# Performance work log

Measured on AMD Instinct MI355X. Metric: run time of the kernel, lower is better.

Reference implementation:

```python
import jax, jax.numpy as jnp
import numpy as np

EPS = 1e-20

def setup_inputs() -> dict:
    key = jax.random.key(0)
    k1, k2, k3, k4, k5 = jax.random.split(key, 5)
    B, S, E, D = 8, 2048, 1024, 1024
    x = jax.random.normal(k1, (B, S, E), dtype=jnp.float32)
    mask = jax.random.randint(k2, (B, S, S), 0, 2, dtype=jnp.int32)
    scale = 1.0 / np.sqrt(E)
    Wq = jax.random.normal(k3, (E, D), dtype=jnp.float32) * scale
    Wk = jax.random.normal(k4, (E, D), dtype=jnp.float32) * scale
    Wv = jax.random.normal(k5, (E, D), dtype=jnp.float32) * scale
    return {"x": x, "mask": mask, "Wq": Wq, "Wk": Wk, "Wv": Wv}

def masked_softmax(scores, mask, axis=-1):
    # non-standard: multiply scores by mask BEFORE softmax, re-mask, renormalize
    w = jax.nn.softmax(scores * mask, axis=axis)
    w = w * mask
    return w / (w.sum(axis, keepdims=True) + EPS)

def reference(x, mask, Wq, Wk, Wv):
    D = Wq.shape[1]
    m = mask.astype(x.dtype)                       # [B,S,S]
    q = jnp.einsum('bse,ed->bsd', x, Wq)
    k = jnp.einsum('bse,ed->bsd', x, Wk)
    v = jnp.einsum('bse,ed->bsd', x, Wv)
    scores = jnp.einsum('bqd,bkd->bqk', q, k) / jnp.sqrt(jnp.asarray(D, x.dtype))
    attn = masked_softmax(scores, m, axis=-1)      # [B,S,S]
    return jnp.einsum('bqk,bkd->bqd', attn, v)
```

## Files before the change

### kernel.cpp

```cpp
#include <hip/hip_runtime.h>
#include <hip/hip_bf16.h>

#define S_LEN 2048
#define E_DIM 1024
#define D_DIM 1024

typedef __bf16 bf16x8 __attribute__((ext_vector_type(8)));
typedef __bf16 bf16x4 __attribute__((ext_vector_type(4)));
typedef float f32x4 __attribute__((ext_vector_type(4)));

__device__ __forceinline__ __bf16 f2bf(float f) {
    unsigned u = __builtin_bit_cast(unsigned, f);
    u += 0x7fffu + ((u >> 16) & 1u);
    unsigned short h = (unsigned short)(u >> 16);
    return __builtin_bit_cast(__bf16, h);
}

__device__ __forceinline__ void async_cp16(void* lds, const void* g) {
    __builtin_amdgcn_global_load_lds(
        (const __attribute__((address_space(1))) void*)g,
        (__attribute__((address_space(3))) void*)lds, 16, 0, 0);
}

#define MFMA_BLOCK()                                                              \
    _Pragma("unroll")                                                             \
    for (int kk = 0; kk < 2; ++kk) {                                              \
        const int kb = kk * 64 + lh * 16;                                         \
        bf16x8 a[4], b[4];                                                        \
        _Pragma("unroll")                                                         \
        for (int m = 0; m < 4; ++m)                                               \
            a[m] = *reinterpret_cast<const bf16x8*>(lsA + (wr*64 + m*16 + rl) * 128 + kb); \
        _Pragma("unroll")                                                         \
        for (int n = 0; n < 4; ++n)                                               \
            b[n] = *reinterpret_cast<const bf16x8*>(lsB + (wc*64 + n*16 + rl) * 128 + kb); \
        _Pragma("unroll")                                                         \
        for (int m = 0; m < 4; ++m)                                               \
            _Pragma("unroll")                                                     \
            for (int n = 0; n < 4; ++n)                                           \
                acc[m][n] = __builtin_amdgcn_mfma_f32_16x16x32_bf16(a[m], b[n], acc[m][n], 0, 0, 0); \
    }

#define STAGE_TILE(lsDst, gBase, row0, kcol, stride)                              \
    _Pragma("unroll")                                                             \
    for (int i_ = 0; i_ < 4; ++i_) {                                              \
        int r_ = wid * 32 + i_ * 8;                                               \
        async_cp16(lsDst + r_ * 128,                                              \
                   gBase + (size_t)((row0) + r_ + lrow) * (stride) + (kcol) + lcol); \
    }

__global__ __launch_bounds__(256) void cvt_x_kernel(
    const float* __restrict__ X, __bf16* __restrict__ Xb)
{
    const int n8 = (8 * S_LEN * E_DIM) / 8;
    for (int i = blockIdx.x * 256 + threadIdx.x; i < n8; i += gridDim.x * 256) {
        const float* p = X + (size_t)i * 8;
        float4 a = *reinterpret_cast<const float4*>(p);
        float4 b = *reinterpret_cast<const float4*>(p + 4);
        bf16x8 h = { f2bf(a.x), f2bf(a.y), f2bf(a.z), f2bf(a.w),
                     f2bf(b.x), f2bf(b.y), f2bf(b.z), f2bf(b.w) };
        *reinterpret_cast<bf16x8*>(Xb + (size_t)i * 8) = h;
    }
}

__global__ __launch_bounds__(256) void wt_kernel(
    const float* __restrict__ Wq, const float* __restrict__ Wk, const float* __restrict__ Wv,
    __bf16* __restrict__ Wt)
{
    __shared__ float t[64][68];
    const int z = blockIdx.z;
    const float* W = (z == 0) ? Wq : (z == 1) ? Wk : Wv;
    const int d0 = blockIdx.x * 64, e0 = blockIdx.y * 64;
    const int tid = threadIdx.x;

    const int er = tid >> 4, dc = (tid & 15) * 4;
    #pragma unroll
    for (int p = 0; p < 4; ++p) {
        int e = p * 16 + er;
        float4 v = *reinterpret_cast<const float4*>(W + (size_t)(e0 + e) * D_DIM + d0 + dc);
        *reinterpret_cast<float4*>(&t[e][dc]) = v;
    }
    __syncthreads();

    const int dl = tid >> 3, ec = (tid & 7) * 8;
    __bf16* O = Wt + (size_t)z * E_DIM * D_DIM;
    #pragma unroll
    for (int p = 0; p < 2; ++p) {
        int d = p * 32 + dl;
        bf16x8 h;
        #pragma unroll
        for (int j = 0; j < 8; ++j) h[j] = f2bf(t[ec + j][d]);
        *reinterpret_cast<bf16x8*>(O + (size_t)(d0 + d) * E_DIM + e0 + ec) = h;
    }
}

__global__ __launch_bounds__(256) void qkv_kernel(
    const __bf16* __restrict__ Xb, const __bf16* __restrict__ Wt,
    __bf16* __restrict__ Qb, __bf16* __restrict__ Kb, __bf16* __restrict__ Vt)
{
    __shared__ __align__(16) char lsA[128 * 128];
    __shared__ __align__(16) char lsB[128 * 128];

    const int nt = blockIdx.x, mt = blockIdx.y, z = blockIdx.z;
    const __bf16* A  = Xb;
    const __bf16* Bm = Wt + (size_t)z * E_DIM * D_DIM;
    const int m0 = mt * 128, n0 = nt * 128;
    const int tid = threadIdx.x, lane = tid & 63, wid = tid >> 6;
    const int wr = wid >> 1, wc = wid & 1;
    const int rl = lane & 15, lh = lane >> 4;
    const int lrow = lane >> 3, lcol = (lane & 7) * 8;

    f32x4 acc[4][4] = {};

    for (int k0 = 0; k0 < E_DIM; k0 += 64) {
        STAGE_TILE(lsA, A,  m0, k0, E_DIM)
        STAGE_TILE(lsB, Bm, n0, k0, E_DIM)
        __syncthreads();
        MFMA_BLOCK()
        __syncthreads();
    }

    if (z < 2) {
        __bf16* O = (z == 0) ? Qb : Kb;
        #pragma unroll
        for (int m = 0; m < 4; ++m) {
            int row = m0 + wr*64 + m*16 + lh*4;
            #pragma unroll
            for (int n = 0; n < 4; ++n) {
                int col = n0 + wc*64 + n*16 + rl;
                #pragma unroll
                for (int r = 0; r < 4; ++r)
                    O[(size_t)(row + r) * D_DIM + col] = f2bf(acc[m][n][r]);
            }
        }
    } else {
        const int bz = m0 >> 11;
        const int srow = m0 & 2047;
        __bf16* O = Vt + (size_t)bz * D_DIM * S_LEN;
        #pragma unroll
        for (int m = 0; m < 4; ++m) {
            int row = srow + wr*64 + m*16 + lh*4;
            #pragma unroll
            for (int n = 0; n < 4; ++n) {
                int col = n0 + wc*64 + n*16 + rl;
                bf16x4 h = { f2bf(acc[m][n][0]), f2bf(acc[m][n][1]),
                             f2bf(acc[m][n][2]), f2bf(acc[m][n][3]) };
                *reinterpret_cast<bf16x4*>(O + (size_t)col * S_LEN + row) = h;
            }
        }
    }
}

__global__ __launch_bounds__(256) void qk_kernel(
    const __bf16* __restrict__ Qb, const __bf16* __restrict__ Kb,
    const int* __restrict__ mask, __bf16* __restrict__ P, float* __restrict__ rowsum)
{
    __shared__ __align__(16) char lsA[128 * 128];
    __shared__ __align__(16) char lsB[128 * 128];

    const int kt = blockIdx.x, qt = blockIdx.y, bz = blockIdx.z;
    const __bf16* A  = Qb + (size_t)bz * S_LEN * D_DIM;
    const __bf16* Bm = Kb + (size_t)bz * S_LEN * D_DIM;
    const int q0 = qt * 128, k0 = kt * 128;
    const int tid = threadIdx.x, lane = tid & 63, wid = tid >> 6;
    const int wr = wid >> 1, wc = wid & 1;
    const int rl = lane & 15, lh = lane >> 4;
    const int lrow = lane >> 3, lcol = (lane & 7) * 8;

    f32x4 acc[4][4] = {};

    for (int d0 = 0; d0 < D_DIM; d0 += 64) {
        STAGE_TILE(lsA, A,  q0, d0, D_DIM)
        STAGE_TILE(lsB, Bm, k0, d0, D_DIM)
        __syncthreads();
        MFMA_BLOCK()
        __syncthreads();
    }

    float rs[4][4] = {};
    const size_t mbase = (size_t)bz * S_LEN * S_LEN;
    #pragma unroll
    for (int m = 0; m < 4; ++m) {
        int row = q0 + wr*64 + m*16 + lh*4;
        #pragma unroll
        for (int n = 0; n < 4; ++n) {
            int col = k0 + wc*64 + n*16 + rl;
            #pragma unroll
            for (int r = 0; r < 4; ++r) {
                float s = acc[m][n][r] * 0.03125f;
                int mk = mask[mbase + (size_t)(row + r) * S_LEN + col];
                float pv = mk ? __expf(s) : 0.0f;
                rs[m][r] += pv;
                P[mbase + (size_t)(row + r) * S_LEN + col] = f2bf(pv);
            }
        }
    }
    #pragma unroll
    for (int m = 0; m < 4; ++m) {
        #pragma unroll
        for (int r = 0; r < 4; ++r) {
            float v = rs[m][r];
            v += __shfl_xor(v, 1);
            v += __shfl_xor(v, 2);
            v += __shfl_xor(v, 4);
            v += __shfl_xor(v, 8);
            if (rl == 0)
                atomicAdd(&rowsum[bz * S_LEN + q0 + wr*64 + m*16 + lh*4 + r], v);
        }
    }
}

__global__ __launch_bounds__(256) void pv_kernel(
    const __bf16* __restrict__ P, const __bf16* __restrict__ Vt,
    const float* __restrict__ rowsum, float* __restrict__ out)
{
    __shared__ __align__(16) char lsA[128 * 128];
    __shared__ __align__(16) char lsB[128 * 128];

    const int dt = blockIdx.x, qt = blockIdx.y, bz = blockIdx.z;
    const __bf16* A  = P  + (size_t)bz * S_LEN * S_LEN;
    const __bf16* Bv = Vt + (size_t)bz * D_DIM * S_LEN;
    const int q0 = qt * 128, d0c = dt * 128;
    const int tid = threadIdx.x, lane = tid & 63, wid = tid >> 6;
    const int wr = wid >> 1, wc = wid & 1;
    const int rl = lane & 15, lh = lane >> 4;
    const int lrow = lane >> 3, lcol = (lane & 7) * 8;

    f32x4 acc[4][4] = {};

    for (int s0 = 0; s0 < S_LEN; s0 += 64) {
        STAGE_TILE(lsA, A,  q0,  s0, S_LEN)
        STAGE_TILE(lsB, Bv, d0c, s0, S_LEN)
        __syncthreads();
        MFMA_BLOCK()
        __syncthreads();
    }

    float* Ob = out + (size_t)bz * S_LEN * D_DIM;
    #pragma unroll
    for (int m = 0; m < 4; ++m) {
        int row = q0 + wr*64 + m*16 + lh*4;
        float inv[4];
        #pragma unroll
        for (int r = 0; r < 4; ++r)
            inv[r] = 1.0f / (rowsum[bz * S_LEN + row + r] + 1e-20f);
        #pragma unroll
        for (int n = 0; n < 4; ++n) {
            int col = d0c + wc*64 + n*16 + rl;
            #pragma unroll
            for (int r = 0; r < 4; ++r)
                Ob[(size_t)(row + r) * D_DIM + col] = acc[m][n][r] * inv[r];
        }
    }
}

extern "C" void kernel_launch(void* const* d_in, const int* in_sizes, int n_in,
                              void* d_out, int out_size, void* d_ws, size_t ws_size,
                              hipStream_t stream) {
    const float* x    = (const float*)d_in[0];
    const int*   mask = (const int*)  d_in[1];
    const float* Wq   = (const float*)d_in[2];
    const float* Wk   = (const float*)d_in[3];
    const float* Wv   = (const float*)d_in[4];
    float* out = (float*)d_out;

    char* ws = (char*)d_ws;
    const size_t SZ_QKV = (size_t)8 * S_LEN * D_DIM * 2;
    const size_t SZ_P   = (size_t)8 * S_LEN * S_LEN * 2;
    __bf16* Qb = (__bf16*)(ws);
    __bf16* Kb = (__bf16*)(ws + SZ_QKV);
    __bf16* Vt = (__bf16*)(ws + 2 * SZ_QKV);
    char*   pbase = ws + 3 * SZ_QKV;
    __bf16* P  = (__bf16*)pbase;
    __bf16* Xb = (__bf16*)pbase;
    __bf16* Wt = (__bf16*)(pbase + (size_t)8 * S_LEN * E_DIM * 2);
    float* rowsum = (float*)(ws + 3 * SZ_QKV + SZ_P);
    const size_t need = 3 * SZ_QKV + SZ_P + (size_t)8 * S_LEN * 4;
    if (ws_size < need) return;

    hipMemsetAsync(rowsum, 0, (size_t)8 * S_LEN * 4, stream);
    cvt_x_kernel<<<2048, 256, 0, stream>>>(x, Xb);
    wt_kernel  <<<dim3(16, 16, 3), 256, 0, stream>>>(Wq, Wk, Wv, Wt);
    qkv_kernel <<<dim3(8, 128, 3), 256, 0, stream>>>(Xb, Wt, Qb, Kb, Vt);
    qk_kernel  <<<dim3(16, 16, 8), 256, 0, stream>>>(Qb, Kb, mask, P, rowsum);
    pv_kernel  <<<dim3(8, 16, 8),  256, 0, stream>>>(P, Vt, rowsum, out);
}
```

Before: 648.0 us.

## Use 256x256 double-buffered swizzled GEMM tiles with 512-thread blocks

Replaces the 128x128 single-buffered GEMM loop shared by the QKV, QK and PV kernels with a 256x256-tile, 8-wave routine. It double-buffers LDS across K-steps with async global-to-LDS loads, XOR-swizzles the LDS layout to avoid bank conflicts, and raises wave priority around the MFMA bursts. The aim is more data reuse per loaded byte and overlap of loads with matrix math. The cost is 128KB of LDS per block and 128 accumulator registers per thread, which may limit occupancy, and fewer blocks are launched, with possible tail effects.

```diff
diff --git a/kernel.cpp b/kernel.cpp
--- a/kernel.cpp
+++ b/kernel.cpp
@@ -16,37 +16,99 @@
     return __builtin_bit_cast(__bf16, h);
 }
 
+__device__ __forceinline__ int swz(int row, int b) {
+    return row * 128 + (b ^ ((row & 7) << 4));
+}
+
 __device__ __forceinline__ void async_cp16(void* lds, const void* g) {
     __builtin_amdgcn_global_load_lds(
         (const __attribute__((address_space(1))) void*)g,
         (__attribute__((address_space(3))) void*)lds, 16, 0, 0);
 }
 
-#define MFMA_BLOCK()                                                              \
-    _Pragma("unroll")                                                             \
-    for (int kk = 0; kk < 2; ++kk) {                                              \
-        const int kb = kk * 64 + lh * 16;                                         \
-        bf16x8 a[4], b[4];                                                        \
-        _Pragma("unroll")                                                         \
-        for (int m = 0; m < 4; ++m)                                               \
-            a[m] = *reinterpret_cast<const bf16x8*>(lsA + (wr*64 + m*16 + rl) * 128 + kb); \
-        _Pragma("unroll")                                                         \
-        for (int n = 0; n < 4; ++n)                                               \
-            b[n] = *reinterpret_cast<const bf16x8*>(lsB + (wc*64 + n*16 + rl) * 128 + kb); \
-        _Pragma("unroll")                                                         \
-        for (int m = 0; m < 4; ++m)                                               \
-            _Pragma("unroll")                                                     \
-            for (int n = 0; n < 4; ++n)                                           \
-                acc[m][n] = __builtin_amdgcn_mfma_f32_16x16x32_bf16(a[m], b[n], acc[m][n], 0, 0, 0); \
-    }
-
-#define STAGE_TILE(lsDst, gBase, row0, kcol, stride)                              \
-    _Pragma("unroll")                                                             \
-    for (int i_ = 0; i_ < 4; ++i_) {                                              \
-        int r_ = wid * 32 + i_ * 8;                                               \
-        async_cp16(lsDst + r_ * 128,                                              \
-                   gBase + (size_t)((row0) + r_ + lrow) * (stride) + (kcol) + lcol); \
-    }
+__device__ __forceinline__ void stage_q64(char* ldsTile, const char* gTile,
+                                          size_t strideB, int q, int tid)
+{
+    const int r   = q * 64 + (tid >> 3);
+    const int cb  = (tid & 7) * 16;
+    const int scb = cb ^ ((r & 7) << 4);
+    async_cp16(ldsTile + q * 8192 + ((tid >> 6) << 10),
+               gTile + (size_t)r * strideB + scb);
+}
+
+template<int QM, int QN>
+__device__ __forceinline__ void mfma_phase(const char* lsA, const char* lsB,
+    int wr, int wc, int rl, int lh, f32x4 (&acc)[8][4])
+{
+    bf16x8 a[4][2]; bf16x8 b[2][2];
+    #pragma unroll
+    for (int m = 0; m < 4; ++m)
+        #pragma unroll
+        for (int ks = 0; ks < 2; ++ks)
+            a[m][ks] = *reinterpret_cast<const bf16x8*>(
+                lsA + swz(wr*128 + QM*64 + m*16 + rl, ks*64 + lh*16));
+    #pragma unroll
+    for (int n = 0; n < 2; ++n)
+        #pragma unroll
+        for (int ks = 0; ks < 2; ++ks)
+            b[n][ks] = *reinterpret_cast<const bf16x8*>(
+                lsB + swz(wc*64 + QN*32 + n*16 + rl, ks*64 + lh*16));
+    __builtin_amdgcn_s_setprio(1);
+    #pragma unroll
+    for (int m = 0; m < 4; ++m)
+        #pragma unroll
+        for (int n = 0; n < 2; ++n)
+            #pragma unroll
+            for (int ks = 0; ks < 2; ++ks)
+                acc[QM*4+m][QN*2+n] = __builtin_amdgcn_mfma_f32_16x16x32_bf16(
+                    a[m][ks], b[n][ks], acc[QM*4+m][QN*2+n], 0, 0, 0);
+    __builtin_amdgcn_s_setprio(0);
+}
+
+__device__ __forceinline__ void gemm256(const char* gA, const char* gB,
+    size_t sA, size_t sB, int nt, char* ls, f32x4 (&acc)[8][4])
+{
+    const int tid = threadIdx.x, lane = tid & 63, wid = tid >> 6;
+    const int wr = wid >> 2, wc = wid & 3;
+    const int rl = lane & 15, lh = lane >> 4;
+    char* bA[2] = { ls,         ls + 65536 };
+    char* bB[2] = { ls + 32768, ls + 98304 };
+
+    #define STGA(t, q) stage_q64(bA[(t) & 1], gA + (size_t)(t) * 128, sA, q, tid)
+    #define STGB(t, q) stage_q64(bB[(t) & 1], gB + (size_t)(t) * 128, sB, q, tid)
+
+    STGA(0,0); STGA(0,1); STGA(0,2); STGA(0,3);
+    STGB(0,0); STGB(0,1); STGB(0,2); STGB(0,3);
+    STGA(1,0); STGA(1,2);
+    asm volatile("s_waitcnt vmcnt(2)" ::: "memory");
+    __builtin_amdgcn_s_barrier();
+    __builtin_amdgcn_sched_barrier(0);
+
+    for (int u = 0; u < nt; ++u) {
+        const char* lA = bA[u & 1]; const char* lB = bB[u & 1];
+        if (u + 1 < nt) {
+            STGA(u+1,1); STGA(u+1,3);
+            STGB(u+1,0); STGB(u+1,1); STGB(u+1,2); STGB(u+1,3);
+        }
+        mfma_phase<0,0>(lA, lB, wr, wc, rl, lh, acc);
+        mfma_phase<0,1>(lA, lB, wr, wc, rl, lh, acc);
+        __builtin_amdgcn_sched_barrier(0);
+        __builtin_amdgcn_s_barrier();
+        __builtin_amdgcn_sched_barrier(0);
+        if (u + 2 < nt) { STGA(u+2,0); STGA(u+2,2); }
+        mfma_phase<1,0>(lA, lB, wr, wc, rl, lh, acc);
+        mfma_phase<1,1>(lA, lB, wr, wc, rl, lh, acc);
+        if (u + 1 < nt) {
+            __builtin_amdgcn_sched_barrier(0);
+            if (u + 2 < nt) { asm volatile("s_waitcnt vmcnt(2)" ::: "memory"); }
+            else            { asm volatile("s_waitcnt vmcnt(0)" ::: "memory"); }
+            __builtin_amdgcn_s_barrier();
+            __builtin_amdgcn_sched_barrier(0);
+        }
+    }
+    #undef STGA
+    #undef STGB
+}
 
 __global__ __launch_bounds__(256) void cvt_x_kernel(
     const float* __restrict__ X, __bf16* __restrict__ Xb)
@@ -93,43 +155,34 @@
     }
 }
 
-__global__ __launch_bounds__(256) void qkv_kernel(
+__global__ __launch_bounds__(512, 2) void qkv_kernel(
     const __bf16* __restrict__ Xb, const __bf16* __restrict__ Wt,
     __bf16* __restrict__ Qb, __bf16* __restrict__ Kb, __bf16* __restrict__ Vt)
 {
-    __shared__ __align__(16) char lsA[128 * 128];
-    __shared__ __align__(16) char lsB[128 * 128];
-
-    const int nt = blockIdx.x, mt = blockIdx.y, z = blockIdx.z;
-    const __bf16* A  = Xb;
-    const __bf16* Bm = Wt + (size_t)z * E_DIM * D_DIM;
-    const int m0 = mt * 128, n0 = nt * 128;
+    __shared__ __align__(16) char ls[131072];
+    const int bx = blockIdx.x, mt = blockIdx.y, z = blockIdx.z;
+    const int m0 = mt * 256, n0 = bx * 256;
+
+    f32x4 acc[8][4] = {};
+    gemm256((const char*)Xb + (size_t)m0 * (E_DIM * 2),
+            (const char*)(Wt + (size_t)z * E_DIM * D_DIM) + (size_t)n0 * (E_DIM * 2),
+            E_DIM * 2, E_DIM * 2, E_DIM / 64, ls, acc);
+
     const int tid = threadIdx.x, lane = tid & 63, wid = tid >> 6;
-    const int wr = wid >> 1, wc = wid & 1;
+    const int wr = wid >> 2, wc = wid & 3;
     const int rl = lane & 15, lh = lane >> 4;
-    const int lrow = lane >> 3, lcol = (lane & 7) * 8;
-
-    f32x4 acc[4][4] = {};
-
-    for (int k0 = 0; k0 < E_DIM; k0 += 64) {
-        STAGE_TILE(lsA, A,  m0, k0, E_DIM)
-        STAGE_TILE(lsB, Bm, n0, k0, E_DIM)
-        __syncthreads();
-        MFMA_BLOCK()
-        __syncthreads();
-    }
 
     if (z < 2) {
         __bf16* O = (z == 0) ? Qb : Kb;
         #pragma unroll
-        for (int m = 0; m < 4; ++m) {
-            int row = m0 + wr*64 + m*16 + lh*4;
-            #pragma unroll
-            for (int n = 0; n < 4; ++n) {
-                int col = n0 + wc*64 + n*16 + rl;
+        for (int mi = 0; mi < 8; ++mi) {
+            int row = m0 + wr*128 + mi*16 + lh*4;
+            #pragma unroll
+            for (int ni = 0; ni < 4; ++ni) {
+                int col = n0 + wc*64 + ni*16 + rl;
                 #pragma unroll
                 for (int r = 0; r < 4; ++r)
-                    O[(size_t)(row + r) * D_DIM + col] = f2bf(acc[m][n][r]);
+                    O[(size_t)(row + r) * D_DIM + col] = f2bf(acc[mi][ni][r]);
             }
         }
     } else {
@@ -137,118 +190,100 @@
         const int srow = m0 & 2047;
         __bf16* O = Vt + (size_t)bz * D_DIM * S_LEN;
         #pragma unroll
-        for (int m = 0; m < 4; ++m) {
-            int row = srow + wr*64 + m*16 + lh*4;
-            #pragma unroll
-            for (int n = 0; n < 4; ++n) {
-                int col = n0 + wc*64 + n*16 + rl;
-                bf16x4 h = { f2bf(acc[m][n][0]), f2bf(acc[m][n][1]),
-                             f2bf(acc[m][n][2]), f2bf(acc[m][n][3]) };
+        for (int mi = 0; mi < 8; ++mi) {
+            int row = srow + wr*128 + mi*16 + lh*4;
+            #pragma unroll
+            for (int ni = 0; ni < 4; ++ni) {
+                int col = n0 + wc*64 + ni*16 + rl;
+                bf16x4 h = { f2bf(acc[mi][ni][0]), f2bf(acc[mi][ni][1]),
+                             f2bf(acc[mi][ni][2]), f2bf(acc[mi][ni][3]) };
                 *reinterpret_cast<bf16x4*>(O + (size_t)col * S_LEN + row) = h;
             }
         }
     }
 }
 
-__global__ __launch_bounds__(256) void qk_kernel(
+__global__ __launch_bounds__(512, 2) void qk_kernel(
     const __bf16* __restrict__ Qb, const __bf16* __restrict__ Kb,
     const int* __restrict__ mask, __bf16* __restrict__ P, float* __restrict__ rowsum)
 {
-    __shared__ __align__(16) char lsA[128 * 128];
-    __shared__ __align__(16) char lsB[128 * 128];
-
+    __shared__ __align__(16) char ls[131072];
     const int kt = blockIdx.x, qt = blockIdx.y, bz = blockIdx.z;
-    const __bf16* A  = Qb + (size_t)bz * S_LEN * D_DIM;
-    const __bf16* Bm = Kb + (size_t)bz * S_LEN * D_DIM;
-    const int q0 = qt * 128, k0 = kt * 128;
+    const int q0 = qt * 256, k0 = kt * 256;
+
+    f32x4 acc[8][4] = {};
+    gemm256((const char*)(Qb + (size_t)bz * S_LEN * D_DIM) + (size_t)q0 * (D_DIM * 2),
+            (const char*)(Kb + (size_t)bz * S_LEN * D_DIM) + (size_t)k0 * (D_DIM * 2),
+            D_DIM * 2, D_DIM * 2, D_DIM / 64, ls, acc);
+
     const int tid = threadIdx.x, lane = tid & 63, wid = tid >> 6;
-    const int wr = wid >> 1, wc = wid & 1;
+    const int wr = wid >> 2, wc = wid & 3;
     const int rl = lane & 15, lh = lane >> 4;
-    const int lrow = lane >> 3, lcol = (lane & 7) * 8;
-
-    f32x4 acc[4][4] = {};
-
-    for (int d0 = 0; d0 < D_DIM; d0 += 64) {
-        STAGE_TILE(lsA, A,  q0, d0, D_DIM)
-        STAGE_TILE(lsB, Bm, k0, d0, D_DIM)
-        __syncthreads();
-        MFMA_BLOCK()
-        __syncthreads();
-    }
-
-    float rs[4][4] = {};
+
+    float rs[8][4] = {};
     const size_t mbase = (size_t)bz * S_LEN * S_LEN;
     #pragma unroll
-    for (int m = 0; m < 4; ++m) {
-        int row = q0 + wr*64 + m*16 + lh*4;
-        #pragma unroll
-        for (int n = 0; n < 4; ++n) {
-            int col = k0 + wc*64 + n*16 + rl;
+    for (int mi = 0; mi < 8; ++mi) {
+        int row = q0 + wr*128 + mi*16 + lh*4;
+        #pragma unroll
+        for (int ni = 0; ni < 4; ++ni) {
+            int col = k0 + wc*64 + ni*16 + rl;
             #pragma unroll
             for (int r = 0; r < 4; ++r) {
-                float s = acc[m][n][r] * 0.03125f;
+                float s = acc[mi][ni][r] * 0.03125f;
                 int mk = mask[mbase + (size_t)(row + r) * S_LEN + col];
                 float pv = mk ? __expf(s) : 0.0f;
-                rs[m][r] += pv;
+                rs[mi][r] += pv;
                 P[mbase + (size_t)(row + r) * S_LEN + col] = f2bf(pv);
             }
         }
     }
     #pragma unroll
-    for (int m = 0; m < 4; ++m) {
+    for (int mi = 0; mi < 8; ++mi) {
         #pragma unroll
         for (int r = 0; r < 4; ++r) {
-            float v = rs[m][r];
+            float v = rs[mi][r];
             v += __shfl_xor(v, 1);
             v += __shfl_xor(v, 2);
             v += __shfl_xor(v, 4);
             v += __shfl_xor(v, 8);
             if (rl == 0)
-                atomicAdd(&rowsum[bz * S_LEN + q0 + wr*64 + m*16 + lh*4 + r], v);
-        }
-    }
-}
-
-__global__ __launch_bounds__(256) void pv_kernel(
+                atomicAdd(&rowsum[bz * S_LEN + q0 + wr*128 + mi*16 + lh*4 + r], v);
+        }
+    }
+}
+
+__global__ __launch_bounds__(512, 2) void pv_kernel(
     const __bf16* __restrict__ P, const __bf16* __restrict__ Vt,
     const float* __restrict__ rowsum, float* __restrict__ out)
 {
-    __shared__ __align__(16) char lsA[128 * 128];
-    __shared__ __align__(16) char lsB[128 * 128];
-
+    __shared__ __align__(16) char ls[131072];
     const int dt = blockIdx.x, qt = blockIdx.y, bz = blockIdx.z;
-    const __bf16* A  = P  + (size_t)bz * S_LEN * S_LEN;
-    const __bf16* Bv = Vt + (size_t)bz * D_DIM * S_LEN;
-    const int q0 = qt * 128, d0c = dt * 128;
+    const int q0 = qt * 256, d0c = dt * 256;
+
+    f32x4 acc[8][4] = {};
+    gemm256((const char*)(P  + (size_t)bz * S_LEN * S_LEN) + (size_t)q0  * (S_LEN * 2),
+            (const char*)(Vt + (size_t)bz * D_DIM * S_LEN) + (size_t)d0c * (S_LEN * 2),
+            S_LEN * 2, S_LEN * 2, S_LEN / 64, ls, acc);
+
     const int tid = threadIdx.x, lane = tid & 63, wid = tid >> 6;
-    const int wr = wid >> 1, wc = wid & 1;
+    const int wr = wid >> 2, wc = wid & 3;
     const int rl = lane & 15, lh = lane >> 4;
-    const int lrow = lane >> 3, lcol = (lane & 7) * 8;
-
-    f32x4 acc[4][4] = {};
-
-    for (int s0 = 0; s0 < S_LEN; s0 += 64) {
-        STAGE_TILE(lsA, A,  q0,  s0, S_LEN)
-        STAGE_TILE(lsB, Bv, d0c, s0, S_LEN)
-        __syncthreads();
-        MFMA_BLOCK()
-        __syncthreads();
-    }
 
     float* Ob = out + (size_t)bz * S_LEN * D_DIM;
     #pragma unroll
-    for (int m = 0; m < 4; ++m) {
-        int row = q0 + wr*64 + m*16 + lh*4;
+    for (int mi = 0; mi < 8; ++mi) {
+        int row = q0 + wr*128 + mi*16 + lh*4;
         float inv[4];
         #pragma unroll
         for (int r = 0; r < 4; ++r)
             inv[r] = 1.0f / (rowsum[bz * S_LEN + row + r] + 1e-20f);
         #pragma unroll
-        for (int n = 0; n < 4; ++n) {
-            int col = d0c + wc*64 + n*16 + rl;
+        for (int ni = 0; ni < 4; ++ni) {
+            int col = d0c + wc*64 + ni*16 + rl;
             #pragma unroll
             for (int r = 0; r < 4; ++r)
-                Ob[(size_t)(row + r) * D_DIM + col] = acc[m][n][r] * inv[r];
+                Ob[(size_t)(row + r) * D_DIM + col] = acc[mi][ni][r] * inv[r];
         }
     }
 }
@@ -280,7 +315,7 @@
     hipMemsetAsync(rowsum, 0, (size_t)8 * S_LEN * 4, stream);
     cvt_x_kernel<<<2048, 256, 0, stream>>>(x, Xb);
     wt_kernel  <<<dim3(16, 16, 3), 256, 0, stream>>>(Wq, Wk, Wv, Wt);
-    qkv_kernel <<<dim3(8, 128, 3), 256, 0, stream>>>(Xb, Wt, Qb, Kb, Vt);
-    qk_kernel  <<<dim3(16, 16, 8), 256, 0, stream>>>(Qb, Kb, mask, P, rowsum);
-    pv_kernel  <<<dim3(8, 16, 8),  256, 0, stream>>>(P, Vt, rowsum, out);
-}
+    qkv_kernel <<<dim3(4, 64, 3), 512, 0, stream>>>(Xb, Wt, Qb, Kb, Vt);
+    qk_kernel  <<<dim3(8, 8, 8),  512, 0, stream>>>(Qb, Kb, mask, P, rowsum);
+    pv_kernel  <<<dim3(4, 8, 8),  512, 0, stream>>>(P, Vt, rowsum, out);
+}
```

After: 710.3 us. 9.6% more time.
